# Kernel tuning notes

Hardware: AMD Instinct MI355X
Metric: run time of the kernel (lower is better)

## Reference

```python
import jax, jax.numpy as jnp
import numpy as np

B, S, D, H = 4, 1024, 1024, 16
DK = D // H


def setup_inputs() -> dict:
    key = jax.random.key(0)
    ks = jax.random.split(key, 14)
    scale = 1.0 / np.sqrt(D)
    inp = {
        "Qx": jax.random.normal(ks[0], (B, S, D), jnp.float32),
        "Kx": jax.random.normal(ks[1], (B, S, D), jnp.float32),
        "Vx": jax.random.normal(ks[2], (B, S, D), jnp.float32),
        "prob_phn": jax.random.uniform(ks[3], (B, S, S), jnp.float32),
        "mask": jax.random.randint(ks[4], (B, S, S), 0, 2, jnp.int32),
        "lambda_val": 1,
        "Wq": jax.random.normal(ks[5], (D, D), jnp.float32) * scale,
        "bq": jnp.zeros((D,), jnp.float32),
        "Wk": jax.random.normal(ks[6], (D, D), jnp.float32) * scale,
        "bk": jnp.zeros((D,), jnp.float32),
        "Wv": jax.random.normal(ks[7], (D, D), jnp.float32) * scale,
        "bv": jnp.zeros((D,), jnp.float32),
        "Wo": jax.random.normal(ks[8], (D, D), jnp.float32) * scale,
        "bo": jnp.zeros((D,), jnp.float32),
    }
    return inp


def _split_heads(x):
    # [B,S,D] -> [B,H,S,DK]
    b, s, _ = x.shape
    return x.reshape(b, s, H, DK).transpose(0, 2, 1, 3)


def reference(Qx, Kx, Vx, prob_phn, mask, lambda_val, Wq, bq, Wk, bk, Wv, bv, Wo, bo):
    q = _split_heads(Qx @ Wq.T + bq)
    k = _split_heads(Kx @ Wk.T + bk)
    v = _split_heads(Vx @ Wv.T + bv)
    scores = jnp.einsum("bhqd,bhkd->bhqk", q, k) / jnp.sqrt(jnp.float32(DK))
    if lambda_val > 0:
        # prob_phn: [B,S,S] -> transpose last two dims, broadcast over heads
        scores = scores - lambda_val * jnp.swapaxes(prob_phn, -2, -1)[:, None]
    scores = jnp.where(mask[:, None] == 0, jnp.float32(-1e9), scores)
    probs = jax.nn.softmax(scores, axis=-1)
    attn = jnp.einsum("bhqk,bhkd->bhqd", probs, v)
    out = attn.transpose(0, 2, 1, 3).reshape(Qx.shape[0], Qx.shape[1], D)
    out = out @ Wo.T + bo
    return (out, mask)
```

## Files before the change

### kernel.cpp

```cpp
#include <hip/hip_runtime.h>
#include <hip/hip_bf16.h>
#include <cstdint>
#include <cstddef>

#define BB 4
#define SS 1024
#define DD 1024
#define HH 16
#define DKK 64

typedef unsigned short u16;
typedef __bf16 bf16_t;
typedef __attribute__((ext_vector_type(8))) bf16_t bf16x8;
typedef __attribute__((ext_vector_type(4))) float floatx4;

static __device__ inline u16 f2bf(float f) {
    union { float f; unsigned u; } v; v.f = f;
    unsigned r = v.u + 0x7fffu + ((v.u >> 16) & 1u);
    return (u16)(r >> 16);
}

static __device__ inline void load16_lds(const void* g, void* l) {
    __builtin_amdgcn_global_load_lds(
        (const __attribute__((address_space(1))) unsigned int*)g,
        (__attribute__((address_space(3))) unsigned int*)l,
        16, 0, 0);
}

static __device__ inline int swz64(int row, int c) { return row * 64 + ((c ^ (row & 7)) * 8); }
static __device__ inline int swz32(int row, int c) { return row * 32 + ((c ^ ((row >> 1) & 3)) * 8); }

__global__ void cvt_all_kernel(const float* __restrict__ Qx, const float* __restrict__ Kx,
                               const float* __restrict__ Vx,
                               const float* __restrict__ Wq, const float* __restrict__ Wk,
                               const float* __restrict__ Wv, const float* __restrict__ Wo,
                               u16* __restrict__ Xq, u16* __restrict__ Xk, u16* __restrict__ Xv,
                               u16* __restrict__ wq, u16* __restrict__ wk,
                               u16* __restrict__ wv, u16* __restrict__ wo)
{
    int u = blockIdx.x * blockDim.x + threadIdx.x;
    const float* src; u16* dst; int off;
    if (u < 3145728) {
        int s = u >> 20;  off = u & 1048575;
        src = (s == 0) ? Qx : (s == 1) ? Kx : Vx;
        dst = (s == 0) ? Xq : (s == 1) ? Xk : Xv;
    } else {
        int v2 = u - 3145728;
        int s = v2 >> 18;  off = v2 & 262143;
        src = (s == 0) ? Wq : (s == 1) ? Wk : (s == 2) ? Wv : Wo;
        dst = (s == 0) ? wq : (s == 1) ? wk : (s == 2) ? wv : wo;
    }
    float4 f = ((const float4*)src)[off];
    ushort4 r;
    r.x = f2bf(f.x); r.y = f2bf(f.y); r.z = f2bf(f.z); r.w = f2bf(f.w);
    ((ushort4*)dst)[off] = r;
}

static __device__ inline float lam_val(const int* p) {
    int v = *p;
    if (v >= -100000 && v <= 100000) return (float)v;
    union { int i; float f; } u; u.i = v; return u.f;
}

__global__ void bias_kernel(const float* __restrict__ prob, const int* __restrict__ mask,
                            const int* __restrict__ lam_p, float* __restrict__ biasT,
                            float* __restrict__ maskOut)
{
    __shared__ float tile[32][33];
    const int b = blockIdx.z;
    const int q0 = blockIdx.x * 32, k0 = blockIdx.y * 32;
    const int tx = threadIdx.x, ty = threadIdx.y;
    tile[ty][tx] = prob[((size_t)b * SS + (k0 + ty)) * SS + (q0 + tx)];
    __syncthreads();
    const float lam = lam_val(lam_p);
    const size_t oidx = ((size_t)b * SS + (q0 + ty)) * SS + (k0 + tx);
    int mi = mask[oidx];
    biasT[oidx] = (mi == 0) ? -1e9f : -lam * tile[tx][ty];
    if (maskOut) maskOut[oidx] = (float)mi;
}

template <int MODE>
static __device__ inline void gemm_body(const u16* __restrict__ A, const u16* __restrict__ W,
                                        const float* __restrict__ bias,
                                        u16* __restrict__ Cb, float* __restrict__ Cf)
{
    constexpr int K = 1024, N = 1024;
    __shared__ __align__(16) u16 As[128 * 32];
    __shared__ __align__(16) u16 Bs[128 * 32];
    const int tid = threadIdx.x;
    const int wv = tid >> 6, ln = tid & 63, l15 = ln & 15, quad = ln >> 4;
    const int mBase = blockIdx.y * 128;
    const int nBase = blockIdx.x * 128;
    const int wm = (wv & 1) * 64, wn = (wv >> 1) * 64;

    const u16* Aptr[2]; const u16* Wptr[2];
    #pragma unroll
    for (int r = 0; r < 2; ++r) {
        int p = r * 256 + wv * 64 + ln;
        int row = p >> 2;
        int c = (p & 3) ^ ((row >> 1) & 3);
        Aptr[r] = A + (size_t)(mBase + row) * K + c * 8;
        Wptr[r] = W + (size_t)(nBase + row) * K + c * 8;
    }

    floatx4 acc[4][4] = {};

    for (int k0 = 0; k0 < K; k0 += 32) {
        __syncthreads();
        #pragma unroll
        for (int r = 0; r < 2; ++r) {
            load16_lds(Aptr[r] + k0, &As[(r * 256 + wv * 64) * 8]);
            load16_lds(Wptr[r] + k0, &Bs[(r * 256 + wv * 64) * 8]);
        }
        __syncthreads();
        bf16x8 af[4], bfr[4];
        #pragma unroll
        for (int i = 0; i < 4; ++i)
            af[i] = *(const bf16x8*)&As[swz32(wm + i * 16 + l15, quad)];
        #pragma unroll
        for (int j = 0; j < 4; ++j)
            bfr[j] = *(const bf16x8*)&Bs[swz32(wn + j * 16 + l15, quad)];
        #pragma unroll
        for (int i = 0; i < 4; ++i)
            #pragma unroll
            for (int j = 0; j < 4; ++j)
                acc[i][j] = __builtin_amdgcn_mfma_f32_16x16x32_bf16(af[i], bfr[j], acc[i][j], 0, 0, 0);
    }

    #pragma unroll
    for (int i = 0; i < 4; ++i) {
        #pragma unroll
        for (int j = 0; j < 4; ++j) {
            int col = nBase + wn + j * 16 + l15;
            float bcol = bias[col];
            if (MODE == 2) {
                int hh = col >> 6, dk = col & 63;
                int row0 = mBase + wm + i * 16 + quad * 4;
                int bb = row0 >> 10, s = row0 & 1023;
                ushort4 v4;
                v4.x = f2bf(acc[i][j][0] + bcol);
                v4.y = f2bf(acc[i][j][1] + bcol);
                v4.z = f2bf(acc[i][j][2] + bcol);
                v4.w = f2bf(acc[i][j][3] + bcol);
                *(ushort4*)&Cb[((size_t)((bb * HH + hh) * DKK) + dk) * SS + s] = v4;
            } else {
                #pragma unroll
                for (int r = 0; r < 4; ++r) {
                    int row = mBase + wm + i * 16 + quad * 4 + r;
                    float v = acc[i][j][r] + bcol;
                    if (MODE == 1) Cf[(size_t)row * N + col] = v;
                    else           Cb[(size_t)row * N + col] = f2bf(v);
                }
            }
        }
    }
}

__global__ __launch_bounds__(256) void gemm_qkv_kernel(
    const u16* __restrict__ Xq, const u16* __restrict__ Xk, const u16* __restrict__ Xv,
    const u16* __restrict__ Wq, const u16* __restrict__ Wk, const u16* __restrict__ Wv,
    const float* __restrict__ bq, const float* __restrict__ bk, const float* __restrict__ bv,
    u16* __restrict__ Cq, u16* __restrict__ Ck, u16* __restrict__ Vtout)
{
    const int z = blockIdx.z;
    if (z == 2) {
        gemm_body<2>(Xv, Wv, bv, Vtout, nullptr);
    } else {
        const u16* A = (z == 0) ? Xq : Xk;
        const u16* W = (z == 0) ? Wq : Wk;
        const float* bias = (z == 0) ? bq : bk;
        u16* C = (z == 0) ? Cq : Ck;
        gemm_body<0>(A, W, bias, C, nullptr);
    }
}

__global__ __launch_bounds__(256) void gemm_out_kernel(
    const u16* __restrict__ A, const u16* __restrict__ W,
    const float* __restrict__ bias, float* __restrict__ Cf)
{
    gemm_body<1>(A, W, bias, nullptr, Cf);
}

__global__ __launch_bounds__(256) void attn_kernel(
    const u16* __restrict__ Qf, const u16* __restrict__ Kf,
    const u16* __restrict__ Vt, const float* __restrict__ biasT,
    u16* __restrict__ Attn)
{
    __shared__ __align__(16) u16 Qs[128 * 64];
    __shared__ __align__(16) u16 Ks[64 * 64];
    __shared__ __align__(16) u16 Vs[64 * 64];
    __shared__ __align__(16) u16 Ps[4][32 * 72];
    const int tid = threadIdx.x;
    const int wv = tid >> 6, ln = tid & 63, l15 = ln & 15, quad = ln >> 4;
    const int qt = blockIdx.x, h = blockIdx.y, b = blockIdx.z;
    const int q0 = qt * 128;

    int row64[2], col64[2];
    #pragma unroll
    for (int r = 0; r < 2; ++r) {
        int p = r * 256 + wv * 64 + ln;
        row64[r] = p >> 3;
        col64[r] = ((p & 7) ^ (row64[r] & 7)) * 8;
    }

    #pragma unroll
    for (int r = 0; r < 4; ++r) {
        int p = r * 256 + wv * 64 + ln;
        int row = p >> 3;
        int c = ((p & 7) ^ (row & 7)) * 8;
        load16_lds(Qf + ((size_t)(b * SS + q0 + row)) * DD + h * DKK + c,
                   &Qs[(r * 256 + wv * 64) * 8]);
    }
    __syncthreads();

    bf16x8 aq[2][2];
    #pragma unroll
    for (int m = 0; m < 2; ++m)
        #pragma unroll
        for (int t = 0; t < 2; ++t)
            aq[m][t] = *(const bf16x8*)&Qs[swz64(wv * 32 + m * 16 + l15, t * 4 + quad)];

    const size_t vt_head = ((size_t)(b * HH + h)) * DKK * SS;
    const u16* Kp[2]; const u16* Vp[2];
    #pragma unroll
    for (int r = 0; r < 2; ++r) {
        Kp[r] = Kf + ((size_t)(b * SS + row64[r])) * DD + h * DKK + col64[r];
        Vp[r] = Vt + vt_head + (size_t)row64[r] * SS + col64[r];
    }

    const float* bp[2][4];
    #pragma unroll
    for (int m = 0; m < 2; ++m)
        #pragma unroll
        for (int r = 0; r < 4; ++r)
            bp[m][r] = biasT + ((size_t)(b * SS + q0 + wv * 32 + m * 16 + quad * 4 + r)) * SS + l15;

    float bv_[2][4][4];
    #pragma unroll
    for (int m = 0; m < 2; ++m)
        #pragma unroll
        for (int j = 0; j < 4; ++j)
            #pragma unroll
            for (int r = 0; r < 4; ++r)
                bv_[m][j][r] = bp[m][r][j * 16];

    floatx4 o[2][4] = {};
    float rsum[2][4] = {};

    for (int kt = 0; kt < 16; ++kt) {
        __syncthreads();
        #pragma unroll
        for (int r = 0; r < 2; ++r) {
            load16_lds(Kp[r], &Ks[(r * 256 + wv * 64) * 8]);
            load16_lds(Vp[r], &Vs[(r * 256 + wv * 64) * 8]);
        }
        __syncthreads();

        floatx4 sfr[2][4];
        #pragma unroll
        for (int j = 0; j < 4; ++j) {
            bf16x8 bk0 = *(const bf16x8*)&Ks[swz64(j * 16 + l15, quad)];
            bf16x8 bk1 = *(const bf16x8*)&Ks[swz64(j * 16 + l15, 4 + quad)];
            #pragma unroll
            for (int m = 0; m < 2; ++m) {
                floatx4 s = {};
                s = __builtin_amdgcn_mfma_f32_16x16x32_bf16(aq[m][0], bk0, s, 0, 0, 0);
                sfr[m][j] = __builtin_amdgcn_mfma_f32_16x16x32_bf16(aq[m][1], bk1, s, 0, 0, 0);
            }
        }

        #pragma unroll
        for (int m = 0; m < 2; ++m)
            #pragma unroll
            for (int j = 0; j < 4; ++j)
                #pragma unroll
                for (int r = 0; r < 4; ++r) {
                    float p = __expf(fmaf(sfr[m][j][r], 0.125f, bv_[m][j][r]));
                    rsum[m][r] += p;
                    Ps[wv][(m * 16 + quad * 4 + r) * 72 + j * 16 + l15] =
                        (u16)(__float_as_uint(p) >> 16);
                }

        #pragma unroll
        for (int r = 0; r < 2; ++r) { Kp[r] += (size_t)64 * DD; Vp[r] += 64; }
        if (kt < 15) {
            #pragma unroll
            for (int m = 0; m < 2; ++m)
                #pragma unroll
                for (int r = 0; r < 4; ++r) {
                    bp[m][r] += 64;
                    #pragma unroll
                    for (int j = 0; j < 4; ++j)
                        bv_[m][j][r] = bp[m][r][j * 16];
                }
        }

        #pragma unroll
        for (int t = 0; t < 2; ++t) {
            bf16x8 ap0 = *(const bf16x8*)&Ps[wv][l15 * 72 + t * 32 + quad * 8];
            bf16x8 ap1 = *(const bf16x8*)&Ps[wv][(16 + l15) * 72 + t * 32 + quad * 8];
            #pragma unroll
            for (int j = 0; j < 4; ++j) {
                bf16x8 bvv = *(const bf16x8*)&Vs[swz64(j * 16 + l15, t * 4 + quad)];
                o[0][j] = __builtin_amdgcn_mfma_f32_16x16x32_bf16(ap0, bvv, o[0][j], 0, 0, 0);
                o[1][j] = __builtin_amdgcn_mfma_f32_16x16x32_bf16(ap1, bvv, o[1][j], 0, 0, 0);
            }
        }
    }

    #pragma unroll
    for (int m = 0; m < 2; ++m)
        #pragma unroll
        for (int r = 0; r < 4; ++r) {
            float s = rsum[m][r];
            s += __shfl_xor(s, 1);
            s += __shfl_xor(s, 2);
            s += __shfl_xor(s, 4);
            s += __shfl_xor(s, 8);
            rsum[m][r] = 1.0f / s;
        }
    #pragma unroll
    for (int m = 0; m < 2; ++m)
        #pragma unroll
        for (int j = 0; j < 4; ++j)
            #pragma unroll
            for (int r = 0; r < 4; ++r) {
                int srow = q0 + wv * 32 + m * 16 + quad * 4 + r;
                int dk = j * 16 + l15;
                Attn[((size_t)(b * SS + srow)) * DD + h * DKK + dk] =
                    f2bf(o[m][j][r] * rsum[m][r]);
            }
}

extern "C" void kernel_launch(void* const* d_in, const int* in_sizes, int n_in,
                              void* d_out, int out_size, void* d_ws, size_t ws_size,
                              hipStream_t stream)
{
    const float* Qx  = (const float*)d_in[0];
    const float* Kx  = (const float*)d_in[1];
    const float* Vx  = (const float*)d_in[2];
    const float* prob = (const float*)d_in[3];
    const int*   mask = (const int*)d_in[4];
    const int*   lam  = (const int*)d_in[5];
    const float* Wq  = (const float*)d_in[6];
    const float* bq  = (const float*)d_in[7];
    const float* Wk  = (const float*)d_in[8];
    const float* bk  = (const float*)d_in[9];
    const float* Wv  = (const float*)d_in[10];
    const float* bv  = (const float*)d_in[11];
    const float* Wo  = (const float*)d_in[12];
    const float* bo  = (const float*)d_in[13];

    char* ws = (char*)d_ws;
    const size_t MB = 1024 * 1024;
    u16*   Xq     = (u16*)(ws + 0 * MB);
    u16*   Xk     = (u16*)(ws + 8 * MB);
    u16*   Xv     = (u16*)(ws + 16 * MB);
    u16*   wq     = (u16*)(ws + 24 * MB);
    u16*   wk     = (u16*)(ws + 26 * MB);
    u16*   wvp    = (u16*)(ws + 28 * MB);
    u16*   wo     = (u16*)(ws + 30 * MB);
    u16*   q_flat = (u16*)(ws + 32 * MB);
    u16*   k_flat = (u16*)(ws + 40 * MB);
    u16*   vt     = (u16*)(ws + 56 * MB);
    float* biasT  = (float*)(ws + 64 * MB);
    u16*   attn   = (u16*)(ws + 80 * MB);

    float* maskOut = (out_size >= 2 * BB * SS * DD) ? (float*)d_out + (size_t)BB * SS * DD
                                                    : nullptr;

    cvt_all_kernel<<<16384, 256, 0, stream>>>(Qx, Kx, Vx, Wq, Wk, Wv, Wo,
                                              Xq, Xk, Xv, wq, wk, wvp, wo);
    bias_kernel<<<dim3(32, 32, 4), dim3(32, 32), 0, stream>>>(prob, mask, lam, biasT, maskOut);
    gemm_qkv_kernel<<<dim3(8, 32, 3), 256, 0, stream>>>(Xq, Xk, Xv, wq, wk, wvp,
                                                        bq, bk, bv, q_flat, k_flat, vt);
    attn_kernel<<<dim3(8, 16, 4), 256, 0, stream>>>(q_flat, k_flat, vt, biasT, attn);
    gemm_out_kernel<<<dim3(8, 32, 1), 256, 0, stream>>>(attn, wo, bo, (float*)d_out);
}
```

Measured before the change: 268.3 us.

## Merge prep kernels, store attention bias as bf16, double-buffer K/V tiles

The two conversion kernels (fp32-to-bf16 for inputs and weights, and the bias transpose/mask) are merged into a single prep launch, and the bias transpose now uses 64x64 tiles. The precomputed attention bias is written as bf16 instead of fp32, which halves its write and read traffic. The attention kernel double-buffers K/V in LDS, issuing the next tile's loads before computing the current one and cutting the syncs per iteration from two to one. Rounding the bias to bf16 loses some precision in the phoneme term. The masked -1e9 value survives the rounding, so masking is unaffected. The ping-pong buffers use more LDS.

```diff
diff --git a/kernel.cpp b/kernel.cpp
--- a/kernel.cpp
+++ b/kernel.cpp
@@ -30,53 +30,64 @@
 static __device__ inline int swz64(int row, int c) { return row * 64 + ((c ^ (row & 7)) * 8); }
 static __device__ inline int swz32(int row, int c) { return row * 32 + ((c ^ ((row >> 1) & 3)) * 8); }
 
-__global__ void cvt_all_kernel(const float* __restrict__ Qx, const float* __restrict__ Kx,
-                               const float* __restrict__ Vx,
-                               const float* __restrict__ Wq, const float* __restrict__ Wk,
-                               const float* __restrict__ Wv, const float* __restrict__ Wo,
-                               u16* __restrict__ Xq, u16* __restrict__ Xk, u16* __restrict__ Xv,
-                               u16* __restrict__ wq, u16* __restrict__ wk,
-                               u16* __restrict__ wv, u16* __restrict__ wo)
-{
-    int u = blockIdx.x * blockDim.x + threadIdx.x;
-    const float* src; u16* dst; int off;
-    if (u < 3145728) {
-        int s = u >> 20;  off = u & 1048575;
-        src = (s == 0) ? Qx : (s == 1) ? Kx : Vx;
-        dst = (s == 0) ? Xq : (s == 1) ? Xk : Xv;
-    } else {
-        int v2 = u - 3145728;
-        int s = v2 >> 18;  off = v2 & 262143;
-        src = (s == 0) ? Wq : (s == 1) ? Wk : (s == 2) ? Wv : Wo;
-        dst = (s == 0) ? wq : (s == 1) ? wk : (s == 2) ? wv : wo;
-    }
-    float4 f = ((const float4*)src)[off];
-    ushort4 r;
-    r.x = f2bf(f.x); r.y = f2bf(f.y); r.z = f2bf(f.z); r.w = f2bf(f.w);
-    ((ushort4*)dst)[off] = r;
-}
-
 static __device__ inline float lam_val(const int* p) {
     int v = *p;
     if (v >= -100000 && v <= 100000) return (float)v;
     union { int i; float f; } u; u.i = v; return u.f;
 }
 
-__global__ void bias_kernel(const float* __restrict__ prob, const int* __restrict__ mask,
-                            const int* __restrict__ lam_p, float* __restrict__ biasT,
-                            float* __restrict__ maskOut)
-{
-    __shared__ float tile[32][33];
-    const int b = blockIdx.z;
-    const int q0 = blockIdx.x * 32, k0 = blockIdx.y * 32;
-    const int tx = threadIdx.x, ty = threadIdx.y;
-    tile[ty][tx] = prob[((size_t)b * SS + (k0 + ty)) * SS + (q0 + tx)];
+__global__ void prep_kernel(const float* __restrict__ Qx, const float* __restrict__ Kx,
+                            const float* __restrict__ Vx,
+                            const float* __restrict__ Wq, const float* __restrict__ Wk,
+                            const float* __restrict__ Wv, const float* __restrict__ Wo,
+                            const float* __restrict__ prob, const int* __restrict__ mask,
+                            const int* __restrict__ lam_p,
+                            u16* __restrict__ Xq, u16* __restrict__ Xk, u16* __restrict__ Xv,
+                            u16* __restrict__ wq, u16* __restrict__ wk,
+                            u16* __restrict__ wv, u16* __restrict__ wo,
+                            u16* __restrict__ biasB, float* __restrict__ maskOut)
+{
+    __shared__ float tile[64][65];
+    const int blk = blockIdx.x, tid = threadIdx.x;
+    if (blk < 16384) {
+        int u = blk * 256 + tid;
+        const float* src; u16* dst; int off;
+        if (u < 3145728) {
+            int s = u >> 20;  off = u & 1048575;
+            src = (s == 0) ? Qx : (s == 1) ? Kx : Vx;
+            dst = (s == 0) ? Xq : (s == 1) ? Xk : Xv;
+        } else {
+            int v2 = u - 3145728;
+            int s = v2 >> 18;  off = v2 & 262143;
+            src = (s == 0) ? Wq : (s == 1) ? Wk : (s == 2) ? Wv : Wo;
+            dst = (s == 0) ? wq : (s == 1) ? wk : (s == 2) ? wv : wo;
+        }
+        float4 f = ((const float4*)src)[off];
+        ushort4 r;
+        r.x = f2bf(f.x); r.y = f2bf(f.y); r.z = f2bf(f.z); r.w = f2bf(f.w);
+        ((ushort4*)dst)[off] = r;
+        return;
+    }
+    int t = blk - 16384;
+    const int b = t >> 8;
+    const int q0 = ((t >> 4) & 15) * 64, k0 = (t & 15) * 64;
+    const int tx = tid & 63, ty = tid >> 6;
+    #pragma unroll
+    for (int r = 0; r < 16; ++r) {
+        int kl = r * 4 + ty;
+        tile[kl][tx] = prob[((size_t)(b * SS + k0 + kl)) * SS + q0 + tx];
+    }
     __syncthreads();
     const float lam = lam_val(lam_p);
-    const size_t oidx = ((size_t)b * SS + (q0 + ty)) * SS + (k0 + tx);
-    int mi = mask[oidx];
-    biasT[oidx] = (mi == 0) ? -1e9f : -lam * tile[tx][ty];
-    if (maskOut) maskOut[oidx] = (float)mi;
+    #pragma unroll
+    for (int r = 0; r < 16; ++r) {
+        int ql = r * 4 + ty;
+        size_t oidx = ((size_t)(b * SS + q0 + ql)) * SS + k0 + tx;
+        int mi = mask[oidx];
+        float bias = (mi == 0) ? -1e9f : -lam * tile[tx][ql];
+        biasB[oidx] = f2bf(bias);
+        if (maskOut) maskOut[oidx] = (float)mi;
+    }
 }
 
 template <int MODE>
@@ -183,12 +194,12 @@
 
 __global__ __launch_bounds__(256) void attn_kernel(
     const u16* __restrict__ Qf, const u16* __restrict__ Kf,
-    const u16* __restrict__ Vt, const float* __restrict__ biasT,
+    const u16* __restrict__ Vt, const u16* __restrict__ biasB,
     u16* __restrict__ Attn)
 {
     __shared__ __align__(16) u16 Qs[128 * 64];
-    __shared__ __align__(16) u16 Ks[64 * 64];
-    __shared__ __align__(16) u16 Vs[64 * 64];
+    __shared__ __align__(16) u16 Ks[2][64 * 64];
+    __shared__ __align__(16) u16 Vs[2][64 * 64];
     __shared__ __align__(16) u16 Ps[4][32 * 72];
     const int tid = threadIdx.x;
     const int wv = tid >> 6, ln = tid & 63, l15 = ln & 15, quad = ln >> 4;
@@ -211,14 +222,6 @@
         load16_lds(Qf + ((size_t)(b * SS + q0 + row)) * DD + h * DKK + c,
                    &Qs[(r * 256 + wv * 64) * 8]);
     }
-    __syncthreads();
-
-    bf16x8 aq[2][2];
-    #pragma unroll
-    for (int m = 0; m < 2; ++m)
-        #pragma unroll
-        for (int t = 0; t < 2; ++t)
-            aq[m][t] = *(const bf16x8*)&Qs[swz64(wv * 32 + m * 16 + l15, t * 4 + quad)];
 
     const size_t vt_head = ((size_t)(b * HH + h)) * DKK * SS;
     const u16* Kp[2]; const u16* Vp[2];
@@ -228,12 +231,26 @@
         Vp[r] = Vt + vt_head + (size_t)row64[r] * SS + col64[r];
     }
 
-    const float* bp[2][4];
+    #pragma unroll
+    for (int r = 0; r < 2; ++r) {
+        load16_lds(Kp[r], &Ks[0][(r * 256 + wv * 64) * 8]);
+        load16_lds(Vp[r], &Vs[0][(r * 256 + wv * 64) * 8]);
+    }
+    __syncthreads();
+
+    bf16x8 aq[2][2];
+    #pragma unroll
+    for (int m = 0; m < 2; ++m)
+        #pragma unroll
+        for (int t = 0; t < 2; ++t)
+            aq[m][t] = *(const bf16x8*)&Qs[swz64(wv * 32 + m * 16 + l15, t * 4 + quad)];
+
+    const u16* bp[2][4];
     #pragma unroll
     for (int m = 0; m < 2; ++m)
         #pragma unroll
         for (int r = 0; r < 4; ++r)
-            bp[m][r] = biasT + ((size_t)(b * SS + q0 + wv * 32 + m * 16 + quad * 4 + r)) * SS + l15;
+            bp[m][r] = biasB + ((size_t)(b * SS + q0 + wv * 32 + m * 16 + quad * 4 + r)) * SS + l15;
 
     float bv_[2][4][4];
     #pragma unroll
@@ -242,25 +259,28 @@
         for (int j = 0; j < 4; ++j)
             #pragma unroll
             for (int r = 0; r < 4; ++r)
-                bv_[m][j][r] = bp[m][r][j * 16];
+                bv_[m][j][r] = __uint_as_float((unsigned)bp[m][r][j * 16] << 16);
 
     floatx4 o[2][4] = {};
     float rsum[2][4] = {};
 
     for (int kt = 0; kt < 16; ++kt) {
-        __syncthreads();
-        #pragma unroll
-        for (int r = 0; r < 2; ++r) {
-            load16_lds(Kp[r], &Ks[(r * 256 + wv * 64) * 8]);
-            load16_lds(Vp[r], &Vs[(r * 256 + wv * 64) * 8]);
-        }
-        __syncthreads();
+        const int cur = kt & 1, nxt = cur ^ 1;
+
+        if (kt < 15) {
+            #pragma unroll
+            for (int r = 0; r < 2; ++r) {
+                Kp[r] += (size_t)64 * DD; Vp[r] += 64;
+                load16_lds(Kp[r], &Ks[nxt][(r * 256 + wv * 64) * 8]);
+                load16_lds(Vp[r], &Vs[nxt][(r * 256 + wv * 64) * 8]);
+            }
+        }
 
         floatx4 sfr[2][4];
         #pragma unroll
         for (int j = 0; j < 4; ++j) {
-            bf16x8 bk0 = *(const bf16x8*)&Ks[swz64(j * 16 + l15, quad)];
-            bf16x8 bk1 = *(const bf16x8*)&Ks[swz64(j * 16 + l15, 4 + quad)];
+            bf16x8 bk0 = *(const bf16x8*)&Ks[cur][swz64(j * 16 + l15, quad)];
+            bf16x8 bk1 = *(const bf16x8*)&Ks[cur][swz64(j * 16 + l15, 4 + quad)];
             #pragma unroll
             for (int m = 0; m < 2; ++m) {
                 floatx4 s = {};
@@ -281,8 +301,6 @@
                         (u16)(__float_as_uint(p) >> 16);
                 }
 
-        #pragma unroll
-        for (int r = 0; r < 2; ++r) { Kp[r] += (size_t)64 * DD; Vp[r] += 64; }
         if (kt < 15) {
             #pragma unroll
             for (int m = 0; m < 2; ++m)
@@ -291,7 +309,7 @@
                     bp[m][r] += 64;
                     #pragma unroll
                     for (int j = 0; j < 4; ++j)
-                        bv_[m][j][r] = bp[m][r][j * 16];
+                        bv_[m][j][r] = __uint_as_float((unsigned)bp[m][r][j * 16] << 16);
                 }
         }
 
@@ -301,11 +319,13 @@
             bf16x8 ap1 = *(const bf16x8*)&Ps[wv][(16 + l15) * 72 + t * 32 + quad * 8];
             #pragma unroll
             for (int j = 0; j < 4; ++j) {
-                bf16x8 bvv = *(const bf16x8*)&Vs[swz64(j * 16 + l15, t * 4 + quad)];
+                bf16x8 bvv = *(const bf16x8*)&Vs[cur][swz64(j * 16 + l15, t * 4 + quad)];
                 o[0][j] = __builtin_amdgcn_mfma_f32_16x16x32_bf16(ap0, bvv, o[0][j], 0, 0, 0);
                 o[1][j] = __builtin_amdgcn_mfma_f32_16x16x32_bf16(ap1, bvv, o[1][j], 0, 0, 0);
             }
         }
+
+        __syncthreads();
     }
 
     #pragma unroll
@@ -363,17 +383,16 @@
     u16*   q_flat = (u16*)(ws + 32 * MB);
     u16*   k_flat = (u16*)(ws + 40 * MB);
     u16*   vt     = (u16*)(ws + 56 * MB);
-    float* biasT  = (float*)(ws + 64 * MB);
+    u16*   biasB  = (u16*)(ws + 64 * MB);
     u16*   attn   = (u16*)(ws + 80 * MB);
 
     float* maskOut = (out_size >= 2 * BB * SS * DD) ? (float*)d_out + (size_t)BB * SS * DD
                                                     : nullptr;
 
-    cvt_all_kernel<<<16384, 256, 0, stream>>>(Qx, Kx, Vx, Wq, Wk, Wv, Wo,
-                                              Xq, Xk, Xv, wq, wk, wvp, wo);
-    bias_kernel<<<dim3(32, 32, 4), dim3(32, 32), 0, stream>>>(prob, mask, lam, biasT, maskOut);
+    prep_kernel<<<17408, 256, 0, stream>>>(Qx, Kx, Vx, Wq, Wk, Wv, Wo, prob, mask, lam,
+                                           Xq, Xk, Xv, wq, wk, wvp, wo, biasB, maskOut);
     gemm_qkv_kernel<<<dim3(8, 32, 3), 256, 0, stream>>>(Xq, Xk, Xv, wq, wk, wvp,
                                                         bq, bk, bv, q_flat, k_flat, vt);
-    attn_kernel<<<dim3(8, 16, 4), 256, 0, stream>>>(q_flat, k_flat, vt, biasT, attn);
+    attn_kernel<<<dim3(8, 16, 4), 256, 0, stream>>>(q_flat, k_flat, vt, biasB, attn);
     gemm_out_kernel<<<dim3(8, 32, 1), 256, 0, stream>>>(attn, wo, bo, (float*)d_out);
 }
```

Result: no change. 267.5 us (-0.3%).
